# Kernel optimization log

Measured on AMD Instinct MI355X. Metric: run time of the kernel, lower is better.

The kernel has to match this reference:

```python
import jax, jax.numpy as jnp
import numpy as np

N, E, D, L = 50000, 625000, 128, 7
EPS = 1e-7   # GENConv message epsilon
T = 1.0      # softmax aggregation temperature (learn_t=False)
NUM_ATOM_FEATS, ATOM_VOCAB = 9, 64
NUM_BOND_FEATS, BOND_VOCAB = 3, 8


def setup_inputs() -> dict:
    key = jax.random.key(0)
    ks = jax.random.split(key, 9)
    x = jax.random.randint(ks[0], (N, NUM_ATOM_FEATS), 0, ATOM_VOCAB, dtype=jnp.int32)
    edge_index = jax.random.randint(ks[1], (2, E), 0, N, dtype=jnp.int32)
    edge_attr = jax.random.randint(ks[2], (E, NUM_BOND_FEATS), 0, BOND_VOCAB, dtype=jnp.int32)
    atom_emb = jax.random.normal(ks[3], (NUM_ATOM_FEATS, ATOM_VOCAB, D), dtype=jnp.float32) * 0.1
    bond_emb = jax.random.normal(ks[4], (NUM_BOND_FEATS, BOND_VOCAB, D), dtype=jnp.float32) * 0.1
    W = jax.random.normal(ks[5], (L, D, D), dtype=jnp.float32) / np.sqrt(D).astype(np.float32)
    b = jnp.zeros((L, D), dtype=jnp.float32)
    ln_gamma = jnp.ones((L, D), dtype=jnp.float32)
    ln_beta = jnp.zeros((L, D), dtype=jnp.float32)
    return dict(x=x, edge_index=edge_index, edge_attr=edge_attr,
                atom_emb=atom_emb, bond_emb=bond_emb, W=W, b=b,
                ln_gamma=ln_gamma, ln_beta=ln_beta)


def _layer_norm(h, g, bta):
    mu = jnp.mean(h, axis=-1, keepdims=True)
    var = jnp.var(h, axis=-1, keepdims=True)
    return (h - mu) * jax.lax.rsqrt(var + 1e-5) * g + bta


def _gen_conv(h, src, dst, edge_emb, Wl, bl):
    # GENConv: msg = relu(x_j + e) + eps; softmax aggregation over dst; Linear(x + m)
    msg = jax.nn.relu(h[src] + edge_emb) + EPS                 # [E, D]
    logits = msg * T
    seg_max = jax.ops.segment_max(logits, dst, num_segments=N)  # [N, D]
    seg_max = jnp.where(jnp.isfinite(seg_max), seg_max, 0.0)    # empty segments
    e = jnp.exp(logits - seg_max[dst])                          # [E, D]
    denom = jax.ops.segment_sum(e, dst, num_segments=N)         # [N, D]
    alpha = e / (denom[dst] + 1e-16)
    m = jax.ops.segment_sum(alpha * msg, dst, num_segments=N)   # [N, D]
    return (h + m) @ Wl + bl


def reference(x, edge_index, edge_attr, atom_emb, bond_emb, W, b, ln_gamma, ln_beta):
    src, dst = edge_index[0], edge_index[1]
    # AtomEncoder: sum of per-feature embedding lookups -> [N, D]
    h = jnp.sum(atom_emb[jnp.arange(NUM_ATOM_FEATS)[None, :], x], axis=1)
    # BondEncoder (conv_encode_edge=False: encoded once) -> [E, D]
    edge_emb = jnp.sum(bond_emb[jnp.arange(NUM_BOND_FEATS)[None, :], edge_attr], axis=1)
    # res+ block, dropout=0 (no-op)
    h = _gen_conv(h, src, dst, edge_emb, W[0], b[0])
    for layer in range(1, L):
        h2 = jax.nn.relu(_layer_norm(h, ln_gamma[layer - 1], ln_beta[layer - 1]))
        h = _gen_conv(h2, src, dst, edge_emb, W[layer], b[layer]) + h
    h = _layer_norm(h, ln_gamma[L - 1], ln_beta[L - 1])
    return h
```

## Files before the change

### kernel.cpp

```cpp
#include <hip/hip_runtime.h>
#include <hip/hip_fp16.h>
#include <math.h>


constexpr int D = 128;
constexpr int NA = 9;
constexpr int NB = 3;

using half8  = __attribute__((ext_vector_type(8))) _Float16;
using floatx4 = __attribute__((ext_vector_type(4))) float;


__global__ void k_hist(const int* __restrict__ dst, int* __restrict__ deg, int E) {
    int e = blockIdx.x * 256 + threadIdx.x;
    if (e < E) atomicAdd(&deg[dst[e]], 1);
}

__global__ void k_scan_a(const int* __restrict__ deg, int* __restrict__ offs,
                         int* __restrict__ bsum, int N) {
    __shared__ int s[256];
    int i = blockIdx.x * 256 + threadIdx.x;
    int v = (i < N) ? deg[i] : 0;
    s[threadIdx.x] = v;
    __syncthreads();
    for (int d = 1; d < 256; d <<= 1) {
        int add = (threadIdx.x >= d) ? s[threadIdx.x - d] : 0;
        __syncthreads();
        s[threadIdx.x] += add;
        __syncthreads();
    }
    if (i < N) offs[i + 1] = s[threadIdx.x];
    if (threadIdx.x == 255) bsum[blockIdx.x] = s[255];
    if (i == 0) offs[0] = 0;
}

__global__ void k_scan_b(const int* __restrict__ bsum, int* __restrict__ bexc, int nb) {
    __shared__ int s[256];
    int t = threadIdx.x;
    int v = (t < nb) ? bsum[t] : 0;
    s[t] = v;
    __syncthreads();
    for (int d = 1; d < 256; d <<= 1) {
        int add = (t >= d) ? s[t - d] : 0;
        __syncthreads();
        s[t] += add;
        __syncthreads();
    }
    if (t < nb) bexc[t] = s[t] - v;
}

__global__ void k_scan_c(int* __restrict__ offs, const int* __restrict__ bexc, int N) {
    int i = blockIdx.x * 256 + threadIdx.x;
    if (i < N) offs[i + 1] += bexc[blockIdx.x];
}

__global__ void k_fill(const int* __restrict__ src, const int* __restrict__ dst,
                       const int* __restrict__ attr, const int* __restrict__ offs,
                       int* __restrict__ cur, int2* __restrict__ recs, int E) {
    int e = blockIdx.x * 256 + threadIdx.x;
    if (e >= E) return;
    int d = dst[e];
    int pos = offs[d] + atomicAdd(&cur[d], 1);
    int cidx = attr[e * 3] * 64 + attr[e * 3 + 1] * 8 + attr[e * 3 + 2];
    recs[pos] = make_int2(src[e], cidx);
}

__global__ void k_comb(const float* __restrict__ bemb, __half* __restrict__ comb16) {
    int gid = blockIdx.x * 256 + threadIdx.x;
    int c = gid >> 5, q = gid & 31;
    int a0 = c >> 6, a1 = (c >> 3) & 7, a2 = c & 7;
    float4 v0 = *(const float4*)(bemb + (a0)*D + q * 4);
    float4 v1 = *(const float4*)(bemb + (8 + a1) * D + q * 4);
    float4 v2 = *(const float4*)(bemb + (16 + a2) * D + q * 4);
    __half2* c2 = (__half2*)comb16;
    c2[c * 64 + q * 2]     = __floats2half2_rn(v0.x + v1.x + v2.x, v0.y + v1.y + v2.y);
    c2[c * 64 + q * 2 + 1] = __floats2half2_rn(v0.z + v1.z + v2.z, v0.w + v1.w + v2.w);
}

__global__ void k_wt(const float* __restrict__ W, __half* __restrict__ Wt16, int total) {
    int o = blockIdx.x * 256 + threadIdx.x;
    if (o >= total) return;
    int l = o >> 14;
    int rem = o & 16383;
    int f = rem >> 7, k = rem & 127;
    Wt16[o] = __float2half_rn(W[(l << 14) + k * 128 + f]);
}


__global__ void k_atom(const int* __restrict__ x, const float* __restrict__ aemb,
                       __half* __restrict__ h16, int N) {
    int wid = (blockIdx.x * blockDim.x + threadIdx.x) >> 6;
    int lane = threadIdx.x & 63;
    if (wid >= N) return;
    const int* xr = x + wid * NA;
    float ax = 0.f, ay = 0.f;
#pragma unroll
    for (int f = 0; f < NA; ++f) {
        int v = xr[f];
        const float2 e = *(const float2*)(aemb + (f * 64 + v) * D + 2 * lane);
        ax += e.x; ay += e.y;
    }
    ((__half2*)h16)[wid * 64 + lane] = __floats2half2_rn(ax, ay);
}


__global__ __launch_bounds__(256) void k_agg(const __half* __restrict__ h16,
                      const int2* __restrict__ recs,
                      const int* __restrict__ offs, const __half* __restrict__ comb16,
                      __half* __restrict__ t16, int N) {
    int wid = (blockIdx.x * blockDim.x + threadIdx.x) >> 6;
    int lane = threadIdx.x & 63;
    if (wid >= N) return;
    int su = __builtin_amdgcn_readfirstlane(offs[wid]);
    int eu = __builtin_amdgcn_readfirstlane(offs[wid + 1]);
    __half2 hm2 = ((const __half2*)h16)[wid * 64 + lane];
    float2 hme = make_float2(__low2float(hm2), __high2float(hm2));
    if (su >= eu) {
        ((__half2*)t16)[wid * 64 + lane] = hm2;
        return;
    }
    constexpr float L2E = 1.4426950408889634f;
    float Sx = 0.f, Sy = 0.f, Wx = 0.f, Wy = 0.f;
    int last = eu - 1;

    const __half2* hrow = (const __half2*)h16 + lane;
    const __half2* crow = (const __half2*)comb16 + lane;

    __half2 ha[4], ca[4], hb[4], cb[4];

    auto loadg = [&](int gb, __half2* hs, __half2* cs) {
#pragma unroll
        for (int i = 0; i < 4; ++i) {
            int idx = gb + i; idx = (idx < last) ? idx : last;
            int2 rr = recs[idx];
            int sj = __builtin_amdgcn_readfirstlane(rr.x);
            int cj = __builtin_amdgcn_readfirstlane(rr.y);
            hs[i] = hrow[sj * 64];
            cs[i] = crow[cj * 64];
        }
    };
    auto compg = [&](int gb, const __half2* hs, const __half2* cs) {
        float px[4], py[4], vx[4], vy[4];
#pragma unroll
        for (int i = 0; i < 4; ++i) {
            float hx = __low2float(hs[i]), hy = __high2float(hs[i]);
            float cx = __low2float(cs[i]), cy = __high2float(cs[i]);
            vx[i] = fmaxf(hx + cx, 0.f) + 1e-7f;
            vy[i] = fmaxf(hy + cy, 0.f) + 1e-7f;
            bool valid = (gb + i) < eu;
            float uxv = valid ? vx[i] * L2E : -INFINITY;
            float uyv = valid ? vy[i] * L2E : -INFINITY;
            px[i] = __builtin_amdgcn_exp2f(uxv);
            py[i] = __builtin_amdgcn_exp2f(uyv);
        }
        Sx += (px[0] + px[1]) + (px[2] + px[3]);
        Sy += (py[0] + py[1]) + (py[2] + py[3]);
        Wx += fmaf(px[0], vx[0], px[1] * vx[1]) + fmaf(px[2], vx[2], px[3] * vx[3]);
        Wy += fmaf(py[0], vy[0], py[1] * vy[1]) + fmaf(py[2], vy[2], py[3] * vy[3]);
    };

    loadg(su, ha, ca);
    loadg(su + 4, hb, cb);
    for (int e = su; e < eu; e += 8) {
        compg(e, ha, ca);
        loadg(e + 8, ha, ca);
        compg(e + 4, hb, cb);
        loadg(e + 12, hb, cb);
    }
    float mx = Wx / (Sx + 1e-16f);
    float my = Wy / (Sy + 1e-16f);
    ((__half2*)t16)[wid * 64 + lane] = __floats2half2_rn(hme.x + mx, hme.y + my);
}


template <int MODE>
__global__ __launch_bounds__(256) void k_gemm(const __half* __restrict__ A16,
                                              const __half* __restrict__ Wt16,
                                              const float* __restrict__ bl,
                                              const __half* __restrict__ res16,
                                              __half* __restrict__ hres16,
                                              const float* __restrict__ g,
                                              const float* __restrict__ bta,
                                              __half* __restrict__ h16,
                                              float* __restrict__ out,
                                              int N, int useRes) {
    int lane = threadIdx.x & 63;
    int wave = threadIdx.x >> 6;
    int quad = lane >> 4, col = lane & 15;
    int node = blockIdx.x * 64 + wave * 16 + col;
    bool nok = node < N;
    int nc = nok ? node : N - 1;

    const __half* arow = A16 + (size_t)nc * 128;
    half8 bfrag[4];
#pragma unroll
    for (int ks = 0; ks < 4; ++ks)
        bfrag[ks] = *(const half8*)(arow + ks * 32 + quad * 8);

    floatx4 acc[8];
#pragma unroll
    for (int ft = 0; ft < 8; ++ft) acc[ft] = (floatx4){0.f, 0.f, 0.f, 0.f};

#pragma unroll
    for (int ft = 0; ft < 8; ++ft) {
        const __half* wrow = Wt16 + (size_t)(ft * 16 + col) * 128;
#pragma unroll
        for (int ks = 0; ks < 4; ++ks) {
            half8 afrag = *(const half8*)(wrow + ks * 32 + quad * 8);
            acc[ft] = __builtin_amdgcn_mfma_f32_16x16x32_f16(afrag, bfrag[ks],
                                                             acc[ft], 0, 0, 0);
        }
    }

    float s = 0.f, ss = 0.f;
#pragma unroll
    for (int ft = 0; ft < 8; ++ft) {
        int f0 = ft * 16 + quad * 4;
        float4 bb = *(const float4*)(bl + f0);
        float o0 = acc[ft][0] + bb.x, o1 = acc[ft][1] + bb.y;
        float o2 = acc[ft][2] + bb.z, o3 = acc[ft][3] + bb.w;
        if (useRes) {
            uint2 rr = *(const uint2*)(res16 + (size_t)nc * 128 + f0);
            __half2 r01 = *(__half2*)&rr.x, r23 = *(__half2*)&rr.y;
            o0 += __low2float(r01); o1 += __high2float(r01);
            o2 += __low2float(r23); o3 += __high2float(r23);
        }
        acc[ft][0] = o0; acc[ft][1] = o1; acc[ft][2] = o2; acc[ft][3] = o3;
        s += (o0 + o1) + (o2 + o3);
        ss += fmaf(o0, o0, o1 * o1) + fmaf(o2, o2, o3 * o3);
        if (MODE == 0 && nok) {
            __half2 h01 = __floats2half2_rn(o0, o1);
            __half2 h23 = __floats2half2_rn(o2, o3);
            uint2 pk = make_uint2(*(unsigned*)&h01, *(unsigned*)&h23);
            *(uint2*)(hres16 + (size_t)node * 128 + f0) = pk;
        }
    }
    s += __shfl_xor(s, 16, 64);  ss += __shfl_xor(ss, 16, 64);
    s += __shfl_xor(s, 32, 64);  ss += __shfl_xor(ss, 32, 64);
    float mu = s * (1.f / 128.f);
    float var = ss * (1.f / 128.f) - mu * mu;
    float rs = rsqrtf(var + 1e-5f);

#pragma unroll
    for (int ft = 0; ft < 8; ++ft) {
        int f0 = ft * 16 + quad * 4;
        float4 gg = *(const float4*)(g + f0);
        float4 bt = *(const float4*)(bta + f0);
        float l0 = (acc[ft][0] - mu) * rs * gg.x + bt.x;
        float l1 = (acc[ft][1] - mu) * rs * gg.y + bt.y;
        float l2 = (acc[ft][2] - mu) * rs * gg.z + bt.z;
        float l3 = (acc[ft][3] - mu) * rs * gg.w + bt.w;
        if (MODE == 0) {
            l0 = fmaxf(l0, 0.f); l1 = fmaxf(l1, 0.f);
            l2 = fmaxf(l2, 0.f); l3 = fmaxf(l3, 0.f);
            if (nok) {
                __half2 h01 = __floats2half2_rn(l0, l1);
                __half2 h23 = __floats2half2_rn(l2, l3);
                uint2 pk = make_uint2(*(unsigned*)&h01, *(unsigned*)&h23);
                *(uint2*)(h16 + (size_t)node * 128 + f0) = pk;
            }
        } else {
            if (nok)
                *(float4*)(out + (size_t)node * 128 + f0) =
                    make_float4(l0, l1, l2, l3);
        }
    }
}


extern "C" void kernel_launch(void* const* d_in, const int* in_sizes, int n_in,
                              void* d_out, int out_size, void* d_ws, size_t ws_size,
                              hipStream_t stream) {
    const int*   x    = (const int*)d_in[0];
    const int*   ei   = (const int*)d_in[1];
    const int*   attr = (const int*)d_in[2];
    const float* aemb = (const float*)d_in[3];
    const float* bemb = (const float*)d_in[4];
    const float* Wf   = (const float*)d_in[5];
    const float* bf   = (const float*)d_in[6];
    const float* gam  = (const float*)d_in[7];
    const float* bet  = (const float*)d_in[8];
    float* out = (float*)d_out;

    const int N = in_sizes[0] / NA;
    const int E = in_sizes[1] / 2;
    const int L = in_sizes[5] / (D * D);

    char* ws = (char*)d_ws;
    size_t o = 0;
    auto carve = [&](size_t bytes) -> void* {
        void* p = (void*)(ws + o);
        o += (bytes + 255) & ~(size_t)255;
        return p;
    };
    __half* hres16 = (__half*)carve((size_t)N * D * 2);
    __half* h16    = (__half*)carve((size_t)N * D * 2);
    __half* t16    = (__half*)carve((size_t)N * D * 2);
    int2*   recs   = (int2*)carve((size_t)E * 8);
    __half* comb16 = (__half*)carve(512 * D * 2);
    __half* Wt16   = (__half*)carve((size_t)L * D * D * 2);
    int*    deg    = (int*)carve((size_t)N * 4);
    int*    cur    = (int*)carve((size_t)N * 4);
    int*    offs   = (int*)carve((size_t)(N + 1) * 4);
    int*    bsum   = (int*)carve(4096);
    int*    bexc   = (int*)carve(4096);

    const int* src = ei;
    const int* dst = ei + E;

    hipMemsetAsync(deg, 0, (size_t)N * 4, stream);
    hipMemsetAsync(cur, 0, (size_t)N * 4, stream);

    int ebl = (E + 255) / 256;
    int nbl = (N + 255) / 256;
    k_comb<<<64, 256, 0, stream>>>(bemb, comb16);
    int wtot = L * D * D;
    k_wt<<<(wtot + 255) / 256, 256, 0, stream>>>(Wf, Wt16, wtot);
    k_hist<<<ebl, 256, 0, stream>>>(dst, deg, E);
    k_scan_a<<<nbl, 256, 0, stream>>>(deg, offs, bsum, N);
    k_scan_b<<<1, 256, 0, stream>>>(bsum, bexc, nbl);
    k_scan_c<<<nbl, 256, 0, stream>>>(offs, bexc, N);
    k_fill<<<ebl, 256, 0, stream>>>(src, dst, attr, offs, cur, recs, E);

    int wbl = (N * 64 + 255) / 256;
    k_atom<<<wbl, 256, 0, stream>>>(x, aemb, h16, N);

    int gbl = (N + 63) / 64;
    for (int l = 0; l < L; ++l) {
        k_agg<<<wbl, 256, 0, stream>>>(h16, recs, offs, comb16, t16, N);
        if (l == L - 1) {
            k_gemm<1><<<gbl, 256, 0, stream>>>(t16, Wt16 + l * D * D, bf + l * D,
                                               hres16, hres16,
                                               gam + l * D, bet + l * D, h16, out,
                                               N, 1);
        } else {
            k_gemm<0><<<gbl, 256, 0, stream>>>(t16, Wt16 + l * D * D, bf + l * D,
                                               hres16, hres16,
                                               gam + l * D, bet + l * D, h16, out,
                                               N, l > 0 ? 1 : 0);
        }
    }
}
```

Baseline: 667.4 us.

## Sort nodes by degree for aggregation and deepen gather prefetch to 16 edges

Builds a degree-sorted node permutation (histogram, scan, fill) so aggregation waves handle nodes in descending degree order, balancing work across waves and blocks. The aggregation kernel also switches from a two-stage 8-edge prefetch to a four-slot 16-edge register queue with sequential accumulation. The permutation costs three small kernels once. It breaks the coalesced, node-ordered writes to t16 and uses more registers, which may lower occupancy.

```diff
diff --git a/kernel.cpp b/kernel.cpp
--- a/kernel.cpp
+++ b/kernel.cpp
@@ -65,6 +65,31 @@
     recs[pos] = make_int2(src[e], cidx);
 }
 
+
+__global__ void k_dhist(const int* __restrict__ deg, int* __restrict__ dbin, int N) {
+    int i = blockIdx.x * 256 + threadIdx.x;
+    if (i >= N) return;
+    int d = deg[i]; d = d < 63 ? d : 63;
+    atomicAdd(&dbin[63 - d], 1);
+}
+
+__global__ void k_dscan(const int* __restrict__ dbin, int* __restrict__ doff) {
+    if (threadIdx.x == 0) {
+        int acc = 0;
+        for (int b = 0; b < 64; ++b) { doff[b] = acc; acc += dbin[b]; }
+    }
+}
+
+__global__ void k_dfill(const int* __restrict__ deg, const int* __restrict__ doff,
+                        int* __restrict__ dcur, int* __restrict__ perm, int N) {
+    int i = blockIdx.x * 256 + threadIdx.x;
+    if (i >= N) return;
+    int d = deg[i]; d = d < 63 ? d : 63;
+    int b = 63 - d;
+    int pos = doff[b] + atomicAdd(&dcur[b], 1);
+    perm[pos] = i;
+}
+
 __global__ void k_comb(const float* __restrict__ bemb, __half* __restrict__ comb16) {
     int gid = blockIdx.x * 256 + threadIdx.x;
     int c = gid >> 5, q = gid & 31;
@@ -107,16 +132,17 @@
 __global__ __launch_bounds__(256) void k_agg(const __half* __restrict__ h16,
                       const int2* __restrict__ recs,
                       const int* __restrict__ offs, const __half* __restrict__ comb16,
+                      const int* __restrict__ perm,
                       __half* __restrict__ t16, int N) {
     int wid = (blockIdx.x * blockDim.x + threadIdx.x) >> 6;
     int lane = threadIdx.x & 63;
     if (wid >= N) return;
-    int su = __builtin_amdgcn_readfirstlane(offs[wid]);
-    int eu = __builtin_amdgcn_readfirstlane(offs[wid + 1]);
-    __half2 hm2 = ((const __half2*)h16)[wid * 64 + lane];
-    float2 hme = make_float2(__low2float(hm2), __high2float(hm2));
+    int nid = perm[wid];
+    int su = __builtin_amdgcn_readfirstlane(offs[nid]);
+    int eu = __builtin_amdgcn_readfirstlane(offs[nid + 1]);
+    __half2 hm2 = ((const __half2*)h16)[nid * 64 + lane];
     if (su >= eu) {
-        ((__half2*)t16)[wid * 64 + lane] = hm2;
+        ((__half2*)t16)[nid * 64 + lane] = hm2;
         return;
     }
     constexpr float L2E = 1.4426950408889634f;
@@ -126,50 +152,56 @@
     const __half2* hrow = (const __half2*)h16 + lane;
     const __half2* crow = (const __half2*)comb16 + lane;
 
-    __half2 ha[4], ca[4], hb[4], cb[4];
-
-    auto loadg = [&](int gb, __half2* hs, __half2* cs) {
+    __half2 hq[16], cq[16];
+
+    auto load4 = [&](int base, int slot) {
 #pragma unroll
         for (int i = 0; i < 4; ++i) {
-            int idx = gb + i; idx = (idx < last) ? idx : last;
+            int idx = base + i; idx = (idx < last) ? idx : last;
             int2 rr = recs[idx];
             int sj = __builtin_amdgcn_readfirstlane(rr.x);
             int cj = __builtin_amdgcn_readfirstlane(rr.y);
-            hs[i] = hrow[sj * 64];
-            cs[i] = crow[cj * 64];
+            hq[slot * 4 + i] = hrow[sj * 64];
+            cq[slot * 4 + i] = crow[cj * 64];
         }
     };
-    auto compg = [&](int gb, const __half2* hs, const __half2* cs) {
-        float px[4], py[4], vx[4], vy[4];
+    auto comp4 = [&](int gb, int slot) {
 #pragma unroll
         for (int i = 0; i < 4; ++i) {
-            float hx = __low2float(hs[i]), hy = __high2float(hs[i]);
-            float cx = __low2float(cs[i]), cy = __high2float(cs[i]);
-            vx[i] = fmaxf(hx + cx, 0.f) + 1e-7f;
-            vy[i] = fmaxf(hy + cy, 0.f) + 1e-7f;
+            float hx = __low2float(hq[slot * 4 + i]), hy = __high2float(hq[slot * 4 + i]);
+            float cx = __low2float(cq[slot * 4 + i]), cy = __high2float(cq[slot * 4 + i]);
+            float vx = fmaxf(hx + cx, 0.f) + 1e-7f;
+            float vy = fmaxf(hy + cy, 0.f) + 1e-7f;
             bool valid = (gb + i) < eu;
-            float uxv = valid ? vx[i] * L2E : -INFINITY;
-            float uyv = valid ? vy[i] * L2E : -INFINITY;
-            px[i] = __builtin_amdgcn_exp2f(uxv);
-            py[i] = __builtin_amdgcn_exp2f(uyv);
-        }
-        Sx += (px[0] + px[1]) + (px[2] + px[3]);
-        Sy += (py[0] + py[1]) + (py[2] + py[3]);
-        Wx += fmaf(px[0], vx[0], px[1] * vx[1]) + fmaf(px[2], vx[2], px[3] * vx[3]);
-        Wy += fmaf(py[0], vy[0], py[1] * vy[1]) + fmaf(py[2], vy[2], py[3] * vy[3]);
+            float ux = valid ? vx * L2E : -INFINITY;
+            float uy = valid ? vy * L2E : -INFINITY;
+            float px = __builtin_amdgcn_exp2f(ux);
+            float py = __builtin_amdgcn_exp2f(uy);
+            Sx += px; Sy += py;
+            Wx = fmaf(px, vx, Wx);
+            Wy = fmaf(py, vy, Wy);
+        }
     };
 
-    loadg(su, ha, ca);
-    loadg(su + 4, hb, cb);
-    for (int e = su; e < eu; e += 8) {
-        compg(e, ha, ca);
-        loadg(e + 8, ha, ca);
-        compg(e + 4, hb, cb);
-        loadg(e + 12, hb, cb);
-    }
+    load4(su, 0);
+    if (su + 4  < eu) load4(su + 4, 1);
+    if (su + 8  < eu) load4(su + 8, 2);
+    if (su + 12 < eu) load4(su + 12, 3);
+
+    int e = su;
+    for (; e + 16 < eu; e += 16) {
+        comp4(e, 0); comp4(e + 4, 1); comp4(e + 8, 2); comp4(e + 12, 3);
+        load4(e + 16, 0); load4(e + 20, 1); load4(e + 24, 2); load4(e + 28, 3);
+    }
+    comp4(e, 0);
+    if (e + 4  < eu) comp4(e + 4, 1);
+    if (e + 8  < eu) comp4(e + 8, 2);
+    if (e + 12 < eu) comp4(e + 12, 3);
+
+    float hx = __low2float(hm2), hy = __high2float(hm2);
     float mx = Wx / (Sx + 1e-16f);
     float my = Wy / (Sy + 1e-16f);
-    ((__half2*)t16)[wid * 64 + lane] = __floats2half2_rn(hme.x + mx, hme.y + my);
+    ((__half2*)t16)[nid * 64 + lane] = __floats2half2_rn(hx + mx, hy + my);
 }
 
 
@@ -302,6 +334,10 @@
     int*    deg    = (int*)carve((size_t)N * 4);
     int*    cur    = (int*)carve((size_t)N * 4);
     int*    offs   = (int*)carve((size_t)(N + 1) * 4);
+    int*    perm   = (int*)carve((size_t)N * 4);
+    int*    dbin   = (int*)carve(256);
+    int*    doff   = (int*)carve(256);
+    int*    dcur   = (int*)carve(256);
     int*    bsum   = (int*)carve(4096);
     int*    bexc   = (int*)carve(4096);
 
@@ -310,6 +346,8 @@
 
     hipMemsetAsync(deg, 0, (size_t)N * 4, stream);
     hipMemsetAsync(cur, 0, (size_t)N * 4, stream);
+    hipMemsetAsync(dbin, 0, 256, stream);
+    hipMemsetAsync(dcur, 0, 256, stream);
 
     int ebl = (E + 255) / 256;
     int nbl = (N + 255) / 256;
@@ -321,13 +359,16 @@
     k_scan_b<<<1, 256, 0, stream>>>(bsum, bexc, nbl);
     k_scan_c<<<nbl, 256, 0, stream>>>(offs, bexc, N);
     k_fill<<<ebl, 256, 0, stream>>>(src, dst, attr, offs, cur, recs, E);
+    k_dhist<<<nbl, 256, 0, stream>>>(deg, dbin, N);
+    k_dscan<<<1, 64, 0, stream>>>(dbin, doff);
+    k_dfill<<<nbl, 256, 0, stream>>>(deg, doff, dcur, perm, N);
 
     int wbl = (N * 64 + 255) / 256;
     k_atom<<<wbl, 256, 0, stream>>>(x, aemb, h16, N);
 
     int gbl = (N + 63) / 64;
     for (int l = 0; l < L; ++l) {
-        k_agg<<<wbl, 256, 0, stream>>>(h16, recs, offs, comb16, t16, N);
+        k_agg<<<wbl, 256, 0, stream>>>(h16, recs, offs, comb16, perm, t16, N);
         if (l == L - 1) {
             k_gemm<1><<<gbl, 256, 0, stream>>>(t16, Wt16 + l * D * D, bf + l * D,
                                                hres16, hres16,
```

New measurement: 987.9 us. 48.0% more time.
